# Kernel tuning notes

Hardware: AMD Instinct MI355X
Metric: run time of the kernel (lower is better)

The kernel has to match this reference:

```python
import jax, jax.numpy as jnp
import numpy as np

T = 2.0  # __init__ arg t (temperature exponent); logits scaled by exp(t)


def setup_inputs() -> dict:
    key = jax.random.key(0)
    k1, k2 = jax.random.split(key)
    N = 4096
    logits_per_image = jax.random.normal(k1, (N, N), dtype=jnp.float32)
    labels = jax.random.randint(k2, (N,), 0, 512, dtype=jnp.int64)
    return {"logits_per_image": logits_per_image, "labels": labels}


def reference(logits_per_image, labels):
    # p[i,j] = softmax over row i of (logits * exp(t))
    N = logits_per_image.shape[0]
    p = jax.nn.softmax(logits_per_image * jnp.exp(jnp.float32(T)), axis=1)
    # mask[i,j] = 1 iff i==j or labels[i] != labels[j]; loss uses
    #   log p[i,i] on the diagonal, mask * log(1 - p[i,j]) off-diagonal.
    diag_term = jnp.sum(jnp.log(jnp.diagonal(p)))
    neq = (labels[:, None] != labels[None, :]).astype(p.dtype)  # zero on diagonal
    off_term = jnp.sum(neq * jnp.log1p(-p))
    return (diag_term + off_term) / N
```

## Files before the change

### kernel.cpp

```cpp
#include <hip/hip_runtime.h>

#define N_DIM 4096
#define SCALE 7.3890560989306495f

__global__ __launch_bounds__(512, 4) void minfonce_kernel(
    const float* __restrict__ logits,
    const int*   __restrict__ labels,
    float*       __restrict__ out)
{
    const int lane = threadIdx.x & 63;
    const int wv   = threadIdx.x >> 6;
    const int row  = (blockIdx.x << 3) + wv;

    __shared__ float sacc[8];

    const float4* rp = reinterpret_cast<const float4*>(logits + (size_t)row * N_DIM);
    const int4*   lp = reinterpret_cast<const int4*>(labels);
    const int     li = labels[row];

    float m16[16];
    float s_all = 0.f, s_mask = 0.f;
#pragma unroll
    for (int g = 0; g < 16; ++g) {
        const float4 t  = rp[lane + 64 * g];
        const int4   lb = lp[lane + 64 * g];
        const float ex = __expf(SCALE * t.x);
        const float ey = __expf(SCALE * t.y);
        const float ez = __expf(SCALE * t.z);
        const float ew = __expf(SCALE * t.w);
        s_all  += (ex + ey) + (ez + ew);
        s_mask += ((lb.x != li ? ex : 0.f) + (lb.y != li ? ey : 0.f))
                + ((lb.z != li ? ez : 0.f) + (lb.w != li ? ew : 0.f));
        m16[g] = fmaxf(fmaxf(ex, ey), fmaxf(ez, ew));
    }
    float emax = m16[0];
#pragma unroll
    for (int g = 1; g < 16; ++g) emax = fmaxf(emax, m16[g]);

#pragma unroll
    for (int off = 1; off < 64; off <<= 1) {
        s_all  += __shfl_xor(s_all, off);
        s_mask += __shfl_xor(s_mask, off);
        emax    = fmaxf(emax, __shfl_xor(emax, off));
    }
    const float S    = s_all;
    const float invS = 1.0f / S;
    const float tau  = 1e-3f * S;
    const float qmax = fmaxf(S - emax, S * 1e-12f) * invS;

    float acc = 0.f;
#pragma unroll
    for (int g = 0; g < 16; ++g) {
        if (m16[g] > tau) {
            const float4 t  = rp[lane + 64 * g];
            const int4   lb = lp[lane + 64 * g];
            { const float ev = __expf(SCALE * t.x);
              if (ev > tau && lb.x != li) {
                  const float p = ev * invS;
                  const float q = (ev == emax) ? qmax : (1.0f - p);
                  acc += __logf(q) + p; } }
            { const float ev = __expf(SCALE * t.y);
              if (ev > tau && lb.y != li) {
                  const float p = ev * invS;
                  const float q = (ev == emax) ? qmax : (1.0f - p);
                  acc += __logf(q) + p; } }
            { const float ev = __expf(SCALE * t.z);
              if (ev > tau && lb.z != li) {
                  const float p = ev * invS;
                  const float q = (ev == emax) ? qmax : (1.0f - p);
                  acc += __logf(q) + p; } }
            { const float ev = __expf(SCALE * t.w);
              if (ev > tau && lb.w != li) {
                  const float p = ev * invS;
                  const float q = (ev == emax) ? qmax : (1.0f - p);
                  acc += __logf(q) + p; } }
        }
    }

    if (lane == 0)
        acc += SCALE * logits[(size_t)row * N_DIM + row] - __logf(S);

#pragma unroll
    for (int off = 1; off < 64; off <<= 1)
        acc += __shfl_xor(acc, off);

    if (lane == 0) sacc[wv] = acc - s_mask * invS;
    __syncthreads();
    if (threadIdx.x == 0) {
        const float total = ((sacc[0] + sacc[1]) + (sacc[2] + sacc[3]))
                          + ((sacc[4] + sacc[5]) + (sacc[6] + sacc[7]));
        atomicAdd(out, total * (1.0f / N_DIM));
    }
}

extern "C" void kernel_launch(void* const* d_in, const int* in_sizes, int n_in,
                              void* d_out, int out_size, void* d_ws, size_t ws_size,
                              hipStream_t stream) {
    const float* logits = (const float*)d_in[0];
    const int*   labels = (const int*)d_in[1];
    float*       out    = (float*)d_out;

    hipMemsetAsync(out, 0, sizeof(float), stream);
    minfonce_kernel<<<N_DIM / 8, 512, 0, stream>>>(logits, labels, out);
}
```

Baseline: 114.6 us.

## Hold row logits in registers, stage labels in LDS, replace atomic with reduce kernel

All 16 float4 logits for each lane are loaded up front behind a sched_barrier and kept in registers, so the second pass no longer reloads them from global memory. The label array is staged once per block in 16 KB of shared memory instead of every wave reading it from global memory twice. The diagonal load is issued early. The memset and atomicAdd are replaced by per-block partial sums in workspace plus a small second reduction kernel, which adds a launch but gives a deterministic sum and more register pressure.

```diff
diff --git a/kernel.cpp b/kernel.cpp
--- a/kernel.cpp
+++ b/kernel.cpp
@@ -3,36 +3,65 @@
 #define N_DIM 4096
 #define SCALE 7.3890560989306495f
 
-__global__ __launch_bounds__(512, 4) void minfonce_kernel(
+__global__ __launch_bounds__(512, 4) void minfonce_rows(
     const float* __restrict__ logits,
     const int*   __restrict__ labels,
-    float*       __restrict__ out)
+    float*       __restrict__ ws)
 {
-    const int lane = threadIdx.x & 63;
-    const int wv   = threadIdx.x >> 6;
+    const int tid  = threadIdx.x;
+    const int lane = tid & 63;
+    const int wv   = tid >> 6;
     const int row  = (blockIdx.x << 3) + wv;
 
+    __shared__ int4  slab[N_DIM / 4];
     __shared__ float sacc[8];
 
+    const int4* lp = reinterpret_cast<const int4*>(labels);
+    slab[tid]       = lp[tid];
+    slab[tid + 512] = lp[tid + 512];
+    const int li = labels[row];
+    __syncthreads();
+
     const float4* rp = reinterpret_cast<const float4*>(logits + (size_t)row * N_DIM);
-    const int4*   lp = reinterpret_cast<const int4*>(labels);
-    const int     li = labels[row];
+
+    const float4 u0  = rp[lane +   0];
+    const float4 u1  = rp[lane +  64];
+    const float4 u2  = rp[lane + 128];
+    const float4 u3  = rp[lane + 192];
+    const float4 u4  = rp[lane + 256];
+    const float4 u5  = rp[lane + 320];
+    const float4 u6  = rp[lane + 384];
+    const float4 u7  = rp[lane + 448];
+    const float4 u8  = rp[lane + 512];
+    const float4 u9  = rp[lane + 576];
+    const float4 u10 = rp[lane + 640];
+    const float4 u11 = rp[lane + 704];
+    const float4 u12 = rp[lane + 768];
+    const float4 u13 = rp[lane + 832];
+    const float4 u14 = rp[lane + 896];
+    const float4 u15 = rp[lane + 960];
+    const float  dv  = logits[(size_t)row * N_DIM + row];
+    __builtin_amdgcn_sched_barrier(0);
 
     float m16[16];
     float s_all = 0.f, s_mask = 0.f;
-#pragma unroll
-    for (int g = 0; g < 16; ++g) {
-        const float4 t  = rp[lane + 64 * g];
-        const int4   lb = lp[lane + 64 * g];
-        const float ex = __expf(SCALE * t.x);
-        const float ey = __expf(SCALE * t.y);
-        const float ez = __expf(SCALE * t.z);
-        const float ew = __expf(SCALE * t.w);
-        s_all  += (ex + ey) + (ez + ew);
-        s_mask += ((lb.x != li ? ex : 0.f) + (lb.y != li ? ey : 0.f))
-                + ((lb.z != li ? ez : 0.f) + (lb.w != li ? ew : 0.f));
-        m16[g] = fmaxf(fmaxf(ex, ey), fmaxf(ez, ew));
-    }
+#define ACCG(G, U) do {                                                \
+        const int4  lb = slab[lane + 64 * (G)];                        \
+        const float ex = __expf(SCALE * U.x);                          \
+        const float ey = __expf(SCALE * U.y);                          \
+        const float ez = __expf(SCALE * U.z);                          \
+        const float ew = __expf(SCALE * U.w);                          \
+        s_all  += (ex + ey) + (ez + ew);                               \
+        s_mask += ((lb.x != li ? ex : 0.f) + (lb.y != li ? ey : 0.f))  \
+                + ((lb.z != li ? ez : 0.f) + (lb.w != li ? ew : 0.f)); \
+        m16[G] = fmaxf(fmaxf(ex, ey), fmaxf(ez, ew));                  \
+    } while (0)
+    ACCG(0, u0);   ACCG(1, u1);   ACCG(2, u2);   ACCG(3, u3);
+    ACCG(4, u4);   ACCG(5, u5);   ACCG(6, u6);   ACCG(7, u7);
+    ACCG(8, u8);   ACCG(9, u9);   ACCG(10, u10); ACCG(11, u11);
+    ACCG(12, u12); ACCG(13, u13); ACCG(14, u14); ACCG(15, u15);
+#undef ACCG
+
     float emax = m16[0];
 #pragma unroll
     for (int g = 1; g < 16; ++g) emax = fmaxf(emax, m16[g]);
@@ -49,48 +78,47 @@
     const float qmax = fmaxf(S - emax, S * 1e-12f) * invS;
 
     float acc = 0.f;
-#pragma unroll
-    for (int g = 0; g < 16; ++g) {
-        if (m16[g] > tau) {
-            const float4 t  = rp[lane + 64 * g];
-            const int4   lb = lp[lane + 64 * g];
-            { const float ev = __expf(SCALE * t.x);
-              if (ev > tau && lb.x != li) {
-                  const float p = ev * invS;
-                  const float q = (ev == emax) ? qmax : (1.0f - p);
-                  acc += __logf(q) + p; } }
-            { const float ev = __expf(SCALE * t.y);
-              if (ev > tau && lb.y != li) {
-                  const float p = ev * invS;
-                  const float q = (ev == emax) ? qmax : (1.0f - p);
-                  acc += __logf(q) + p; } }
-            { const float ev = __expf(SCALE * t.z);
-              if (ev > tau && lb.z != li) {
-                  const float p = ev * invS;
-                  const float q = (ev == emax) ? qmax : (1.0f - p);
-                  acc += __logf(q) + p; } }
-            { const float ev = __expf(SCALE * t.w);
-              if (ev > tau && lb.w != li) {
-                  const float p = ev * invS;
-                  const float q = (ev == emax) ? qmax : (1.0f - p);
-                  acc += __logf(q) + p; } }
-        }
-    }
-
-    if (lane == 0)
-        acc += SCALE * logits[(size_t)row * N_DIM + row] - __logf(S);
+#define FIX1(X, L) {                                                   \
+        const float ev = __expf(SCALE * (X));                          \
+        if (ev > tau && (L) != li) {                                   \
+            const float p = ev * invS;                                 \
+            const float q = (ev == emax) ? qmax : (1.0f - p);          \
+            acc += __logf(q) + p; } }
+#define FIXG(G, U) if (m16[G] > tau) {                                 \
+        const int4 lb = slab[lane + 64 * (G)];                         \
+        FIX1(U.x, lb.x) FIX1(U.y, lb.y) FIX1(U.z, lb.z) FIX1(U.w, lb.w) }
+    FIXG(0, u0);   FIXG(1, u1);   FIXG(2, u2);   FIXG(3, u3);
+    FIXG(4, u4);   FIXG(5, u5);   FIXG(6, u6);   FIXG(7, u7);
+    FIXG(8, u8);   FIXG(9, u9);   FIXG(10, u10); FIXG(11, u11);
+    FIXG(12, u12); FIXG(13, u13); FIXG(14, u14); FIXG(15, u15);
+#undef FIXG
+#undef FIX1
 
 #pragma unroll
     for (int off = 1; off < 64; off <<= 1)
         acc += __shfl_xor(acc, off);
-
-    if (lane == 0) sacc[wv] = acc - s_mask * invS;
+    if (lane == 0)
+        sacc[wv] = acc + (SCALE * dv - __logf(S)) - s_mask * invS;
     __syncthreads();
-    if (threadIdx.x == 0) {
+    if (tid == 0) {
         const float total = ((sacc[0] + sacc[1]) + (sacc[2] + sacc[3]))
                           + ((sacc[4] + sacc[5]) + (sacc[6] + sacc[7]));
-        atomicAdd(out, total * (1.0f / N_DIM));
+        ws[blockIdx.x] = total;
     }
+}
+
+__global__ __launch_bounds__(64) void minfonce_reduce(
+    const float* __restrict__ ws,
+    float*       __restrict__ out)
+{
+    const int lane = threadIdx.x;
+    float a = 0.f;
+#pragma unroll
+    for (int i = 0; i < 8; ++i) a += ws[lane + 64 * i];
+#pragma unroll
+    for (int off = 1; off < 64; off <<= 1)
+        a += __shfl_xor(a, off);
+    if (lane == 0) out[0] = a * (1.0f / N_DIM);
 }
 
 extern "C" void kernel_launch(void* const* d_in, const int* in_sizes, int n_in,
@@ -99,7 +127,8 @@
     const float* logits = (const float*)d_in[0];
     const int*   labels = (const int*)d_in[1];
     float*       out    = (float*)d_out;
+    float*       ws     = (float*)d_ws;
 
-    hipMemsetAsync(out, 0, sizeof(float), stream);
-    minfonce_kernel<<<N_DIM / 8, 512, 0, stream>>>(logits, labels, out);
+    minfonce_rows<<<N_DIM / 8, 512, 0, stream>>>(logits, labels, ws);
+    minfonce_reduce<<<1, 64, 0, stream>>>(ws, out);
 }
```

New measurement: 96.84 us. 1.18x faster.
